# Optimization experiments

Measured on AMD Instinct MI355X. Metric: run time of the kernel, lower is better.

## Reference

```python
import jax, jax.numpy as jnp
import numpy as np

B, N, D, H = 8, 1024, 768, 12
DH = D // H
DFF = 4 * D
EPS = 1e-5


def setup_inputs() -> dict:
    key = jax.random.key(0)
    ks = jax.random.split(key, 16)
    s = 0.02
    return {
        "x": jax.random.normal(ks[0], (B, N, D), jnp.float32),
        "ln1_g": jnp.ones((D,), jnp.float32),
        "ln1_b": jnp.zeros((D,), jnp.float32),
        "wqkv": jax.random.normal(ks[1], (D, 3 * D), jnp.float32) * s,
        "bqkv": jnp.zeros((3 * D,), jnp.float32),
        "wo": jax.random.normal(ks[2], (D, D), jnp.float32) * s,
        "bo": jnp.zeros((D,), jnp.float32),
        "rel_bias": jax.random.normal(ks[3], (H, N, N), jnp.float32) * s,
        "ln2_g": jnp.ones((D,), jnp.float32),
        "ln2_b": jnp.zeros((D,), jnp.float32),
        "w1": jax.random.normal(ks[4], (D, DFF), jnp.float32) * s,
        "b1": jnp.zeros((DFF,), jnp.float32),
        "w2": jax.random.normal(ks[5], (DFF, D), jnp.float32) * s,
        "b2": jnp.zeros((D,), jnp.float32),
    }


def _layer_norm(x, g, b):
    mu = jnp.mean(x, axis=-1, keepdims=True)
    var = jnp.mean(jnp.square(x - mu), axis=-1, keepdims=True)
    return (x - mu) * jax.lax.rsqrt(var + EPS) * g + b


def reference(x, ln1_g, ln1_b, wqkv, bqkv, wo, bo, rel_bias, ln2_g, ln2_b, w1, b1, w2, b2):
    # --- pre-norm self-attention with relative position bias + residual ---
    h = _layer_norm(x, ln1_g, ln1_b)
    qkv = h @ wqkv + bqkv                      # [B, N, 3D]
    qkv = qkv.reshape(B, N, 3, H, DH)
    q, k, v = qkv[:, :, 0], qkv[:, :, 1], qkv[:, :, 2]  # each [B, N, H, DH]
    scale = 1.0 / jnp.sqrt(jnp.asarray(DH, x.dtype))
    scores = jnp.einsum("bnhd,bmhd->bhnm", q, k) * scale + rel_bias[None]
    attn = jax.nn.softmax(scores, axis=-1)
    ctx = jnp.einsum("bhnm,bmhd->bnhd", attn, v).reshape(B, N, D)
    x = ctx @ wo + bo + x
    # --- pre-norm FFN (GELU) + residual ---
    h = _layer_norm(x, ln2_g, ln2_b)
    h = jax.nn.gelu(h @ w1 + b1)
    x = h @ w2 + b2 + x
    return x
```

## Files before the change

### kernel.cpp

```cpp
#include <hip/hip_runtime.h>
#include <hip/hip_bf16.h>
#include <math.h>

#define D_MODEL 768
#define NTOK    8192
#define SEQ     1024
#define NH      12
#define DHD     64
#define DFF     3072

typedef __attribute__((ext_vector_type(8)))  __bf16 bf16x8;
typedef __attribute__((ext_vector_type(4)))  float  f32x4;
typedef __attribute__((ext_vector_type(16))) float  f32x16;
typedef __attribute__((ext_vector_type(4)))  unsigned short us4;

typedef const __attribute__((address_space(1))) void g_void;
typedef __attribute__((address_space(3))) void lds_void;

__device__ __forceinline__ unsigned short f2bf(float f) {
  unsigned u = __float_as_uint(f);
  u += 0x7fffu + ((u >> 16) & 1u);
  return (unsigned short)(u >> 16);
}

__device__ __forceinline__ f32x16 mfma32(bf16x8 a, bf16x8 b, f32x16 c) {
  return __builtin_amdgcn_mfma_f32_32x32x16_bf16(a, b, c, 0, 0, 0);
}

__device__ __forceinline__ void gload_lds16(const unsigned short* g, unsigned short* l) {
  __builtin_amdgcn_global_load_lds((g_void*)g, (lds_void*)l, 16, 0, 0);
}

__device__ __forceinline__ void plswap(unsigned &a, unsigned &b) {
  asm("v_permlane32_swap_b32 %0, %1" : "+v"(a), "+v"(b));
}
__device__ __forceinline__ bf16x8 mk8(unsigned a, unsigned b, unsigned c, unsigned d) {
  union { unsigned u[4]; bf16x8 v; } t;
  t.u[0] = a; t.u[1] = b; t.u[2] = c; t.u[3] = d;
  return t.v;
}

__device__ __forceinline__ void ln_row(const float* __restrict__ x,
                                       const float* __restrict__ gam,
                                       const float* __restrict__ bet,
                                       unsigned short* __restrict__ out,
                                       size_t row, int lane) {
  const float* xr = x + row * D_MODEL;
  f32x4 v[3];
#pragma unroll
  for (int c = 0; c < 3; ++c) v[c] = *(const f32x4*)(xr + c * 256 + lane * 4);
  float s = 0.f;
#pragma unroll
  for (int c = 0; c < 3; ++c)
#pragma unroll
    for (int j = 0; j < 4; ++j) s += v[c][j];
#pragma unroll
  for (int o = 32; o; o >>= 1) s += __shfl_xor(s, o);
  const float mu = s * (1.0f / D_MODEL);
  float vs = 0.f;
#pragma unroll
  for (int c = 0; c < 3; ++c)
#pragma unroll
    for (int j = 0; j < 4; ++j) { float d = v[c][j] - mu; vs += d * d; }
#pragma unroll
  for (int o = 32; o; o >>= 1) vs += __shfl_xor(vs, o);
  const float rs = rsqrtf(vs * (1.0f / D_MODEL) + 1e-5f);
  unsigned short* orow = out + row * D_MODEL;
#pragma unroll
  for (int c = 0; c < 3; ++c) {
    us4 o4;
#pragma unroll
    for (int j = 0; j < 4; ++j) {
      int idx = c * 256 + lane * 4 + j;
      o4[j] = f2bf((v[c][j] - mu) * rs * gam[idx] + bet[idx]);
    }
    *(us4*)(orow + c * 256 + lane * 4) = o4;
  }
}

__global__ __launch_bounds__(256)
void ln_kernel(const float* __restrict__ x, const float* __restrict__ gam,
               const float* __restrict__ bet, unsigned short* __restrict__ out) {
  ln_row(x, gam, bet, out, (size_t)blockIdx.x * 4 + (threadIdx.x >> 6), threadIdx.x & 63);
}

__device__ __forceinline__ void wtrans_body(const float* __restrict__ W,
                                            unsigned short* __restrict__ Wt,
                                            int K, int Nc, int bx, int by, int tid) {
  __shared__ float t[32][33];
  const int tx = tid & 31, ty = tid >> 5;
  const int nb = bx * 32, kb = by * 32;
#pragma unroll
  for (int i = 0; i < 4; ++i)
    t[ty + 8 * i][tx] = W[(size_t)(kb + ty + 8 * i) * Nc + nb + tx];
  __syncthreads();
#pragma unroll
  for (int i = 0; i < 4; ++i)
    Wt[(size_t)(nb + ty + 8 * i) * K + kb + tx] = f2bf(t[tx][ty + 8 * i]);
}

__device__ __forceinline__ void brelayout_body(const float* __restrict__ rel,
                                               unsigned short* __restrict__ bF,
                                               int blk, int tid) {
  const int gw = blk * 4 + (tid >> 6);
  const int lane = tid & 63;
  const int ktg = gw & 31, qt = (gw >> 5) & 31, h = gw >> 10;
  const int q = qt * 32 + (lane & 31), hi = lane >> 5;
  const float* src = rel + ((size_t)h * SEQ + q) * SEQ + ktg * 32 + 4 * hi;
  const float L2E = 1.4426950408889634f;
  unsigned ow[8];
#pragma unroll
  for (int g = 0; g < 4; ++g) {
    f32x4 v = *(const f32x4*)(src + g * 8);
    asm("v_cvt_pk_bf16_f32 %0, %1, %2" : "=v"(ow[2 * g])     : "v"(v[0] * L2E), "v"(v[1] * L2E));
    asm("v_cvt_pk_bf16_f32 %0, %1, %2" : "=v"(ow[2 * g + 1]) : "v"(v[2] * L2E), "v"(v[3] * L2E));
  }
  unsigned short* dst = bF + (((size_t)gw) * 64 + lane) * 16;
  *(uint4*)(dst)     = make_uint4(ow[0], ow[1], ow[2], ow[3]);
  *(uint4*)(dst + 8) = make_uint4(ow[4], ow[5], ow[6], ow[7]);
}

#define WP0 1728
#define WP1 (WP0 + 576)
#define WP2 (WP1 + 2304)
#define WP3 (WP2 + 2304)
#define WP4 (WP3 + 3072)
#define WP5 (WP4 + 2048)
__global__ __launch_bounds__(256)
void wprep_kernel(const float* __restrict__ wqkv, unsigned short* __restrict__ wqkvT,
                  const float* __restrict__ wo, unsigned short* __restrict__ woT,
                  const float* __restrict__ w1, unsigned short* __restrict__ w1T,
                  const float* __restrict__ w2, unsigned short* __restrict__ w2T,
                  const float* __restrict__ rel, unsigned short* __restrict__ biasF,
                  const float* __restrict__ x, const float* __restrict__ ln1_g,
                  const float* __restrict__ ln1_b, unsigned short* __restrict__ hbuf) {
  const int b = blockIdx.x, tid = threadIdx.x;
  if (b < WP0)      wtrans_body(wqkv, wqkvT, 768, 2304, b % 72, b / 72, tid);
  else if (b < WP1) wtrans_body(wo, woT, 768, 768, (b - WP0) % 24, (b - WP0) / 24, tid);
  else if (b < WP2) wtrans_body(w1, w1T, 768, 3072, (b - WP1) % 96, (b - WP1) / 96, tid);
  else if (b < WP3) wtrans_body(w2, w2T, 3072, 768, (b - WP2) % 24, (b - WP2) / 24, tid);
  else if (b < WP4) brelayout_body(rel, biasF, b - WP3, tid);
  else              ln_row(x, ln1_g, ln1_b, hbuf,
                           (size_t)(b - WP4) * 4 + (tid >> 6), tid & 63);
}

#define MODE_QKV  0
#define MODE_PROJ 1
#define MODE_FFN1 2
#define MODE_FFN2 3

template <int MODE>
__global__ __launch_bounds__(256)
void gemm_bt(const unsigned short* __restrict__ A, const unsigned short* __restrict__ Bt,
             int K, const float* __restrict__ bias, const float* __restrict__ resid,
             float* __restrict__ outF, unsigned short* __restrict__ o0,
             unsigned short* __restrict__ o1, unsigned short* __restrict__ o2) {
  __shared__ alignas(16) unsigned short smem[2][2][128 * 64];
  const int tid = threadIdx.x;
  const int w = tid >> 6, lane = tid & 63;
  const int l31 = lane & 31, hi = lane >> 5;
  const int wm = w >> 1, wn = w & 1;
  const int nwg = gridDim.x * gridDim.y;
  const int bid0 = blockIdx.y * gridDim.x + blockIdx.x;
  const int cpx = nwg >> 3;
  const int bid = (bid0 & 7) * cpx + (bid0 >> 3);
  const int bx = bid % gridDim.x, by = bid / gridDim.x;
  const size_t m0 = (size_t)by * 128;
  const size_t n0 = (size_t)bx * 128;
  const unsigned short* gA = A + m0 * K;
  const unsigned short* gB = Bt + n0 * K;

  const int r8 = lane >> 3;
  const int u8 = lane & 7;
  const int ucol = (u8 ^ r8) * 8;

  f32x16 acc[2][2];
#pragma unroll
  for (int i = 0; i < 2; ++i)
#pragma unroll
    for (int j = 0; j < 2; ++j) acc[i][j] = (f32x16)(0.f);
  const int nk = K >> 6;

  auto stage = [&](int buf, int kt) {
#pragma unroll
    for (int g = 0; g < 4; ++g) {
      const int rowb = w * 32 + g * 8;
      gload_lds16(gA + (size_t)(rowb + r8) * K + kt * 64 + ucol, &smem[0][buf][rowb * 64]);
      gload_lds16(gB + (size_t)(rowb + r8) * K + kt * 64 + ucol, &smem[1][buf][rowb * 64]);
    }
  };

  const int swr = l31 & 7;
  const int rA = (wm * 64 + l31) * 64;
  const int rB = (wn * 64 + l31) * 64;

  stage(0, 0);
  __syncthreads();
  for (int kt = 0; kt < nk; ++kt) {
    const int buf = kt & 1;
    if (kt + 1 < nk) stage(buf ^ 1, kt + 1);
    bf16x8 af[2][4], bf[2][4];
#pragma unroll
    for (int mt = 0; mt < 2; ++mt)
#pragma unroll
      for (int ks = 0; ks < 4; ++ks) {
        af[mt][ks] = *(const bf16x8*)&smem[0][buf][rA + mt * 2048 + (((ks * 2 + hi) ^ swr) * 8)];
        bf[mt][ks] = *(const bf16x8*)&smem[1][buf][rB + mt * 2048 + (((ks * 2 + hi) ^ swr) * 8)];
      }
#pragma unroll
    for (int mt = 0; mt < 2; ++mt)
#pragma unroll
      for (int nt = 0; nt < 2; ++nt)
#pragma unroll
        for (int ks = 0; ks < 4; ++ks)
          acc[mt][nt] = mfma32(af[mt][ks], bf[nt][ks], acc[mt][nt]);
    __syncthreads();
  }

  if constexpr (MODE == MODE_QKV) {
    if (bx >= 12) {
      unsigned short* tb = &smem[0][0][0];
#pragma unroll
      for (int mt = 0; mt < 2; ++mt)
#pragma unroll
        for (int nt = 0; nt < 2; ++nt)
#pragma unroll
          for (int r = 0; r < 16; ++r) {
            const int nl = wn * 64 + nt * 32 + l31;
            const int ml = wm * 64 + mt * 32 + (r & 3) + 8 * (r >> 2) + 4 * hi;
            tb[nl * 136 + ml] = f2bf(acc[mt][nt][r] + bias[(int)n0 + nl]);
          }
      __syncthreads();
      const int rr = tid & 127, half = tid >> 7;
      const int n2 = ((int)n0 - 1536) + rr;
      const int hh = n2 >> 6, dh = n2 & 63;
      const int b2 = (int)(m0 >> 10), nq0 = (int)(m0 & 1023);
      unsigned short* dst = o2 + ((size_t)(b2 * NH + hh) * DHD + dh) * SEQ + nq0 + half * 64;
      const unsigned short* src = tb + rr * 136 + half * 64;
#pragma unroll
      for (int i = 0; i < 4; ++i)
        *(uint4*)(dst + i * 8) = *(const uint4*)(src + i * 8);
      return;
    }
  }

#pragma unroll
  for (int mt = 0; mt < 2; ++mt) {
#pragma unroll
    for (int nt = 0; nt < 2; ++nt) {
#pragma unroll
      for (int r = 0; r < 16; ++r) {
        const int m = (int)m0 + wm * 64 + mt * 32 + (r & 3) + 8 * (r >> 2) + 4 * hi;
        const int n = (int)n0 + wn * 64 + nt * 32 + l31;
        float v = acc[mt][nt][r] + bias[n];
        if constexpr (MODE == MODE_QKV) {
          const int b = m >> 10, nq = m & 1023;
          if (n < 768) {
            const int h = n >> 6, dh = n & 63;
            o0[(((size_t)(b * NH + h)) * SEQ + nq) * DHD + dh] =
                f2bf(v * 0.1803368801111244f);
          } else {
            const int n2 = n - 768, h = n2 >> 6, dh = n2 & 63;
            o1[(((size_t)(b * NH + h)) * SEQ + nq) * DHD + dh] = f2bf(v);
          }
        } else if constexpr (MODE == MODE_PROJ) {
          const size_t off = (size_t)m * D_MODEL + n;
          outF[off] = v + resid[off];
        } else if constexpr (MODE == MODE_FFN1) {
          const float t = v * v;
          const float s = fmaf(-0.10295276f, t, -2.3022164f);
          const float e = __builtin_amdgcn_exp2f(v * s);
          o0[(size_t)m * DFF + n] = f2bf(v * __builtin_amdgcn_rcpf(1.0f + e));
        } else {
          const size_t off = (size_t)m * D_MODEL + n;
          outF[off] = v + resid[off];
        }
      }
    }
  }
}

__global__ __launch_bounds__(256, 4)
void attn_kernel(const unsigned short* __restrict__ q, const unsigned short* __restrict__ k,
                 const unsigned short* __restrict__ vt, const unsigned short* __restrict__ bF,
                 unsigned short* __restrict__ ctx) {
  __shared__ alignas(16) unsigned short kv[2][16][64 * 8];
  const int tid = threadIdx.x, w = tid >> 6, lane = tid & 63;
  const int l31 = lane & 31, hi = lane >> 5;
  const int bid = (blockIdx.x & 7) * 96 + (blockIdx.x >> 3);
  const int bh = bid >> 3, qblk = bid & 7;
  const int b = bh / NH, h = bh % NH;
  const int q0w = qblk * 128 + w * 32;
  const unsigned short* qp = q + (size_t)bh * SEQ * DHD;
  const unsigned short* kp = k + (size_t)bh * SEQ * DHD;
  const unsigned short* vp = vt + (size_t)bh * DHD * SEQ;
  const unsigned short* bfp = bF + ((((size_t)(h * 32 + qblk * 4 + w)) * 32) * 64 + lane) * 16;

  bf16x8 Qf[4];
#pragma unroll
  for (int ds = 0; ds < 4; ++ds)
    Qf[ds] = *(const bf16x8*)(qp + (size_t)(q0w + l31) * DHD + ds * 16 + hi * 8);

  f32x16 o[2];
#pragma unroll
  for (int dt = 0; dt < 2; ++dt) o[dt] = (f32x16)(0.f);
  float mrun = -INFINITY, lrun = 0.f;

  auto stage = [&](int buf, int kb) {
    if (w < 2) {
      const unsigned short* g0 = kp + (size_t)(kb * 64 + w * 32 + l31) * DHD + hi * 8;
#pragma unroll
      for (int ds = 0; ds < 4; ++ds)
        gload_lds16(g0 + ds * 16, &kv[buf][w * 4 + ds][0]);
    } else {
      const int dt = w - 2;
      const unsigned short* g0 = vp + (size_t)(dt * 32 + l31) * SEQ + kb * 64 + hi * 8;
#pragma unroll
      for (int kh = 0; kh < 4; ++kh)
        gload_lds16(g0 + kh * 16, &kv[buf][8 + dt * 4 + kh][0]);
    }
  };

  stage(0, 0);
  __syncthreads();
  for (int kb = 0; kb < SEQ / 64; ++kb) {
    const int buf = kb & 1;
    if (kb + 1 < SEQ / 64) stage(buf ^ 1, kb + 1);

    f32x16 s0 = (f32x16)(0.f), s1 = (f32x16)(0.f);
    __builtin_amdgcn_s_setprio(1);
#pragma unroll
    for (int ds = 0; ds < 4; ++ds) {
      bf16x8 kf0 = *(const bf16x8*)&kv[buf][ds][lane * 8];
      s0 = mfma32(kf0, Qf[ds], s0);
      bf16x8 kf1 = *(const bf16x8*)&kv[buf][4 + ds][lane * 8];
      s1 = mfma32(kf1, Qf[ds], s1);
    }
    __builtin_amdgcn_s_setprio(0);

    const unsigned short* bb = bfp + (size_t)(kb * 2) * 64 * 16;
    uint4 a0 = *(const uint4*)(bb),            a1 = *(const uint4*)(bb + 8);
    uint4 c0 = *(const uint4*)(bb + 64 * 16),  c1 = *(const uint4*)(bb + 64 * 16 + 8);
    unsigned uw0[8] = {a0.x, a0.y, a0.z, a0.w, a1.x, a1.y, a1.z, a1.w};
    unsigned uw1[8] = {c0.x, c0.y, c0.z, c0.w, c1.x, c1.y, c1.z, c1.w};
    float p0[16], p1[16];
#pragma unroll
    for (int j = 0; j < 8; ++j) {
      p0[2 * j]     = s0[2 * j]     + __uint_as_float(uw0[j] << 16);
      p0[2 * j + 1] = s0[2 * j + 1] + __uint_as_float(uw0[j] & 0xffff0000u);
      p1[2 * j]     = s1[2 * j]     + __uint_as_float(uw1[j] << 16);
      p1[2 * j + 1] = s1[2 * j + 1] + __uint_as_float(uw1[j] & 0xffff0000u);
    }

    float pmax = p0[0];
#pragma unroll
    for (int i = 1; i < 16; ++i) pmax = fmaxf(pmax, p0[i]);
#pragma unroll
    for (int i = 0; i < 16; ++i) pmax = fmaxf(pmax, p1[i]);
    if (!__all(pmax - mrun <= 11.0f)) {
      float pm = fmaxf(pmax, __shfl_xor(pmax, 32));
      const float mn = fmaxf(mrun, pm);
      const float al = __builtin_amdgcn_exp2f(mrun - mn);
      mrun = mn;
      lrun *= al;
#pragma unroll
      for (int dt = 0; dt < 2; ++dt)
#pragma unroll
        for (int r = 0; r < 16; ++r) o[dt][r] *= al;
    }
#pragma unroll
    for (int i = 0; i < 16; ++i) { p0[i] = __builtin_amdgcn_exp2f(p0[i] - mrun); lrun += p0[i]; }
#pragma unroll
    for (int i = 0; i < 16; ++i) { p1[i] = __builtin_amdgcn_exp2f(p1[i] - mrun); lrun += p1[i]; }

    unsigned wpk[16];
#pragma unroll
    for (int i = 0; i < 8; ++i) {
      asm("v_cvt_pk_bf16_f32 %0, %1, %2" : "=v"(wpk[i])     : "v"(p0[2 * i]), "v"(p0[2 * i + 1]));
      asm("v_cvt_pk_bf16_f32 %0, %1, %2" : "=v"(wpk[8 + i]) : "v"(p1[2 * i]), "v"(p1[2 * i + 1]));
    }
    plswap(wpk[0], wpk[2]);   plswap(wpk[1], wpk[3]);
    plswap(wpk[4], wpk[6]);   plswap(wpk[5], wpk[7]);
    plswap(wpk[8], wpk[10]);  plswap(wpk[9], wpk[11]);
    plswap(wpk[12], wpk[14]); plswap(wpk[13], wpk[15]);
    bf16x8 pf[4];
    pf[0] = mk8(wpk[0], wpk[1], wpk[2], wpk[3]);
    pf[1] = mk8(wpk[4], wpk[5], wpk[6], wpk[7]);
    pf[2] = mk8(wpk[8], wpk[9], wpk[10], wpk[11]);
    pf[3] = mk8(wpk[12], wpk[13], wpk[14], wpk[15]);

    __builtin_amdgcn_s_setprio(1);
#pragma unroll
    for (int dt = 0; dt < 2; ++dt)
#pragma unroll
      for (int kh = 0; kh < 4; ++kh) {
        bf16x8 vf = *(const bf16x8*)&kv[buf][8 + dt * 4 + kh][lane * 8];
        o[dt] = mfma32(vf, pf[kh], o[dt]);
      }
    __builtin_amdgcn_s_setprio(0);

    __syncthreads();
  }

  lrun += __shfl_xor(lrun, 32);
  const float inv = 1.0f / lrun;
  unsigned short* crow = ctx + ((size_t)b * SEQ + q0w + l31) * D_MODEL + h * DHD;
#pragma unroll
  for (int dt = 0; dt < 2; ++dt)
#pragma unroll
    for (int g = 0; g < 4; ++g) {
      us4 ov;
#pragma unroll
      for (int j = 0; j < 4; ++j) ov[j] = f2bf(o[dt][4 * g + j] * inv);
      *(us4*)(crow + dt * 32 + g * 8 + 4 * hi) = ov;
    }
}

extern "C" void kernel_launch(void* const* d_in, const int* in_sizes, int n_in,
                              void* d_out, int out_size, void* d_ws, size_t ws_size,
                              hipStream_t stream) {
  (void)in_sizes; (void)n_in; (void)out_size; (void)ws_size;
  const float* x     = (const float*)d_in[0];
  const float* ln1_g = (const float*)d_in[1];
  const float* ln1_b = (const float*)d_in[2];
  const float* wqkv  = (const float*)d_in[3];
  const float* bqkv  = (const float*)d_in[4];
  const float* wo    = (const float*)d_in[5];
  const float* bo    = (const float*)d_in[6];
  const float* rel   = (const float*)d_in[7];
  const float* ln2_g = (const float*)d_in[8];
  const float* ln2_b = (const float*)d_in[9];
  const float* w1    = (const float*)d_in[10];
  const float* b1    = (const float*)d_in[11];
  const float* w2    = (const float*)d_in[12];
  const float* b2    = (const float*)d_in[13];
  float* out = (float*)d_out;

  char* p = (char*)d_ws;
  auto take = [&](size_t bytes) {
    void* r = (void*)p;
    p += (bytes + 255) & ~(size_t)255;
    return r;
  };
  unsigned short* hbuf  = (unsigned short*)take((size_t)NTOK * D_MODEL * 2);
  unsigned short* wqkvT = (unsigned short*)take((size_t)2304 * 768 * 2);
  unsigned short* woT   = (unsigned short*)take((size_t)768 * 768 * 2);
  unsigned short* w1T   = (unsigned short*)take((size_t)3072 * 768 * 2);
  unsigned short* w2T   = (unsigned short*)take((size_t)768 * 3072 * 2);
  unsigned short* qbuf  = (unsigned short*)take((size_t)8 * NH * SEQ * DHD * 2);
  unsigned short* kbuf  = (unsigned short*)take((size_t)8 * NH * SEQ * DHD * 2);
  unsigned short* vtbuf = (unsigned short*)take((size_t)8 * NH * SEQ * DHD * 2);
  unsigned short* ctxb  = (unsigned short*)take((size_t)NTOK * D_MODEL * 2);
  unsigned short* h1buf = (unsigned short*)take((size_t)NTOK * DFF * 2);
  unsigned short* biasF = h1buf;

  wprep_kernel<<<WP5, 256, 0, stream>>>(wqkv, wqkvT, wo, woT, w1, w1T, w2, w2T,
                                        rel, biasF, x, ln1_g, ln1_b, hbuf);
  gemm_bt<MODE_QKV><<<dim3(2304 / 128, NTOK / 128), 256, 0, stream>>>(
      hbuf, wqkvT, 768, bqkv, nullptr, nullptr, qbuf, kbuf, vtbuf);
  attn_kernel<<<8 * NH * (SEQ / 128), 256, 0, stream>>>(qbuf, kbuf, vtbuf, biasF, ctxb);
  gemm_bt<MODE_PROJ><<<dim3(768 / 128, NTOK / 128), 256, 0, stream>>>(
      ctxb, woT, 768, bo, x, out, nullptr, nullptr, nullptr);
  ln_kernel<<<NTOK / 4, 256, 0, stream>>>(out, ln2_g, ln2_b, hbuf);
  gemm_bt<MODE_FFN1><<<dim3(DFF / 128, NTOK / 128), 256, 0, stream>>>(
      hbuf, w1T, 768, b1, nullptr, nullptr, h1buf, nullptr, nullptr);
  gemm_bt<MODE_FFN2><<<dim3(768 / 128, NTOK / 128), 256, 0, stream>>>(
      h1buf, w2T, 3072, b2, out, out, nullptr, nullptr, nullptr);
}
```

Before: 256.1 us.

## Load GEMM B operand directly to registers, halve LDS, raise occupancy

The B (weight) tile no longer goes through LDS. Each wave loads its B fragments straight from global memory into registers, prefetching the next k-tile after the MFMAs, so only the A tile is double-buffered in shared memory. This halves LDS use, which together with launch_bounds(256,4) is meant to allow more resident workgroups, and it wraps the MFMA block in s_setprio. In exchange the B reads are uncoalesced 16-byte per-lane loads that are repeated across the waves that share wn, and the prefetch in flight adds register pressure.

```diff
diff --git a/kernel.cpp b/kernel.cpp
--- a/kernel.cpp
+++ b/kernel.cpp
@@ -150,12 +150,12 @@
 #define MODE_FFN2 3
 
 template <int MODE>
-__global__ __launch_bounds__(256)
+__global__ __launch_bounds__(256, 4)
 void gemm_bt(const unsigned short* __restrict__ A, const unsigned short* __restrict__ Bt,
              int K, const float* __restrict__ bias, const float* __restrict__ resid,
              float* __restrict__ outF, unsigned short* __restrict__ o0,
              unsigned short* __restrict__ o1, unsigned short* __restrict__ o2) {
-  __shared__ alignas(16) unsigned short smem[2][2][128 * 64];
+  __shared__ alignas(16) unsigned short smem[(MODE == MODE_QKV) ? 17408 : 16384];
   const int tid = threadIdx.x;
   const int w = tid >> 6, lane = tid & 63;
   const int l31 = lane & 31, hi = lane >> 5;
@@ -185,41 +185,52 @@
 #pragma unroll
     for (int g = 0; g < 4; ++g) {
       const int rowb = w * 32 + g * 8;
-      gload_lds16(gA + (size_t)(rowb + r8) * K + kt * 64 + ucol, &smem[0][buf][rowb * 64]);
-      gload_lds16(gB + (size_t)(rowb + r8) * K + kt * 64 + ucol, &smem[1][buf][rowb * 64]);
-    }
+      gload_lds16(gA + (size_t)(rowb + r8) * K + kt * 64 + ucol,
+                  &smem[buf * 8192 + rowb * 64]);
+    }
+  };
+
+  bf16x8 breg[8];
+  auto loadB = [&](int kt) {
+#pragma unroll
+    for (int nt = 0; nt < 2; ++nt)
+#pragma unroll
+      for (int ks = 0; ks < 4; ++ks)
+        breg[nt * 4 + ks] = *(const bf16x8*)(
+            gB + (size_t)(wn * 64 + nt * 32 + l31) * K + kt * 64 + (ks * 2 + hi) * 8);
   };
 
   const int swr = l31 & 7;
   const int rA = (wm * 64 + l31) * 64;
-  const int rB = (wn * 64 + l31) * 64;
 
   stage(0, 0);
+  loadB(0);
   __syncthreads();
   for (int kt = 0; kt < nk; ++kt) {
     const int buf = kt & 1;
     if (kt + 1 < nk) stage(buf ^ 1, kt + 1);
-    bf16x8 af[2][4], bf[2][4];
-#pragma unroll
-    for (int mt = 0; mt < 2; ++mt)
-#pragma unroll
-      for (int ks = 0; ks < 4; ++ks) {
-        af[mt][ks] = *(const bf16x8*)&smem[0][buf][rA + mt * 2048 + (((ks * 2 + hi) ^ swr) * 8)];
-        bf[mt][ks] = *(const bf16x8*)&smem[1][buf][rB + mt * 2048 + (((ks * 2 + hi) ^ swr) * 8)];
-      }
-#pragma unroll
-    for (int mt = 0; mt < 2; ++mt)
+#pragma unroll
+    for (int mt = 0; mt < 2; ++mt) {
+      bf16x8 af[4];
+#pragma unroll
+      for (int ks = 0; ks < 4; ++ks)
+        af[ks] = *(const bf16x8*)&smem[buf * 8192 + rA + mt * 2048 +
+                                       (((ks * 2 + hi) ^ swr) * 8)];
+      __builtin_amdgcn_s_setprio(1);
 #pragma unroll
       for (int nt = 0; nt < 2; ++nt)
 #pragma unroll
         for (int ks = 0; ks < 4; ++ks)
-          acc[mt][nt] = mfma32(af[mt][ks], bf[nt][ks], acc[mt][nt]);
+          acc[mt][nt] = mfma32(af[ks], breg[nt * 4 + ks], acc[mt][nt]);
+      __builtin_amdgcn_s_setprio(0);
+    }
+    if (kt + 1 < nk) loadB(kt + 1);
     __syncthreads();
   }
 
   if constexpr (MODE == MODE_QKV) {
     if (bx >= 12) {
-      unsigned short* tb = &smem[0][0][0];
+      unsigned short* tb = &smem[0];
 #pragma unroll
       for (int mt = 0; mt < 2; ++mt)
 #pragma unroll
```

Result: slower. 502.3 us (+96.2%).
